# Kernel tuning notes

Measured on AMD Instinct MI355X. Metric: run time of the kernel, lower is better.

## Reference

```python
import jax, jax.numpy as jnp
import numpy as np

D_MODEL = 1024
NUM_HEADS = 16
HEAD_DIM = D_MODEL // NUM_HEADS


def setup_inputs() -> dict:
    key = jax.random.key(0)
    ks = jax.random.split(key, 9)
    B, S = 2, 2048
    s = 1.0 / np.sqrt(D_MODEL)
    inp = {
        "x": jax.random.normal(ks[0], (B, S, D_MODEL), dtype=jnp.float32),
        "Wq": jax.random.normal(ks[1], (D_MODEL, D_MODEL), dtype=jnp.float32) * s,
        "bq": jnp.zeros((D_MODEL,), dtype=jnp.float32),
        "Wk": jax.random.normal(ks[2], (D_MODEL, D_MODEL), dtype=jnp.float32) * s,
        "bk": jnp.zeros((D_MODEL,), dtype=jnp.float32),
        "Wv": jax.random.normal(ks[3], (D_MODEL, D_MODEL), dtype=jnp.float32) * s,
        "bv": jnp.zeros((D_MODEL,), dtype=jnp.float32),
        "Wo": jax.random.normal(ks[4], (D_MODEL, D_MODEL), dtype=jnp.float32) * s,
        "bo": jnpp if False else jnp.zeros((D_MODEL,), dtype=jnp.float32),
    }
    return inp


def reference(x, Wq, bq, Wk, bk, Wv, bv, Wo, bo):
    B, S, D = x.shape
    H, hd = NUM_HEADS, HEAD_DIM
    # QKV projections (Linear: x @ W^T + b), split into heads -> [B,H,S,hd]
    q = (x @ Wq.T + bq).reshape(B, S, H, hd).transpose(0, 2, 1, 3)
    k = (x @ Wk.T + bk).reshape(B, S, H, hd).transpose(0, 2, 1, 3)
    v = (x @ Wv.T + bv).reshape(B, S, H, hd).transpose(0, 2, 1, 3)
    # scores [B,H,S,S]
    scores = jnp.einsum('bhqd,bhkd->bhqk', q, k) / jnp.sqrt(jnp.float32(hd))
    p = jax.nn.softmax(scores, axis=-1)
    out = jnp.einsum('bhqk,bhkd->bhqd', p, v)  # [B,H,S,hd]
    out = out.transpose(0, 2, 1, 3).reshape(B, S, D)
    return out @ Wo.T + bo
```

## Files before the change

kernel.cpp:

```cpp
#include <hip/hip_runtime.h>
#include <hip/hip_bf16.h>
#include <math.h>

typedef __bf16 bf16;
typedef unsigned short u16;
typedef __bf16 bf16x8 __attribute__((ext_vector_type(8)));
typedef __bf16 bf16x4 __attribute__((ext_vector_type(4)));
typedef short  s16x4  __attribute__((ext_vector_type(4)));
typedef float  f32x4  __attribute__((ext_vector_type(4)));

#define D_MODEL 1024
#define NHEAD   16
#define HD      64
#define BATCH   2
#define SEQ     2048
#define MTOT    (BATCH*SEQ)

#define EXPSCALE 0.18033688011116016f

__device__ __forceinline__ void async16(const void* g, void* l) {
    __builtin_amdgcn_global_load_lds(
        (__attribute__((address_space(1))) unsigned int*)g,
        (__attribute__((address_space(3))) unsigned int*)l,
        16, 0, 0);
}

__device__ __forceinline__ f32x4 mfma16(s16x4 a, s16x4 b, f32x4 c) {
    return __builtin_amdgcn_mfma_f32_16x16x16bf16_1k(a, b, c, 0, 0, 0);
}

__global__ __launch_bounds__(256) void cast_kernel(
    const float* __restrict__ x,
    const float* __restrict__ wq, const float* __restrict__ wk,
    const float* __restrict__ wv, const float* __restrict__ wo,
    bf16* __restrict__ xb, bf16* __restrict__ wqb, bf16* __restrict__ wkb,
    bf16* __restrict__ wvb, bf16* __restrict__ wob)
{
    const int z = blockIdx.y;
    const float* src;
    bf16* dst;
    int n;
    if (z == 0)      { src = x;  dst = xb;  n = MTOT * D_MODEL; }
    else if (z == 1) { src = wq; dst = wqb; n = D_MODEL * D_MODEL; }
    else if (z == 2) { src = wk; dst = wkb; n = D_MODEL * D_MODEL; }
    else if (z == 3) { src = wv; dst = wvb; n = D_MODEL * D_MODEL; }
    else             { src = wo; dst = wob; n = D_MODEL * D_MODEL; }

    int i = (blockIdx.x * 256 + threadIdx.x) * 8;
    if (i >= n) return;
    float4 a = *(const float4*)(src + i);
    float4 b = *(const float4*)(src + i + 4);
    bf16x8 o;
    o[0] = (bf16)a.x; o[1] = (bf16)a.y; o[2] = (bf16)a.z; o[3] = (bf16)a.w;
    o[4] = (bf16)b.x; o[5] = (bf16)b.y; o[6] = (bf16)b.z; o[7] = (bf16)b.w;
    *(bf16x8*)(dst + i) = o;
}

__device__ __forceinline__ void gemm_core(const bf16* __restrict__ A,
                                          const bf16* __restrict__ W,
                                          int m0, int n0,
                                          f32x4 acc[4][4],
                                          u16* lA, u16* lB)
{
    const int tid  = threadIdx.x;
    const int lane = tid & 63;
    const int wave = tid >> 6;
    const int wr   = wave >> 1;
    const int wc   = wave & 1;
    const int fr   = lane & 15;
    const int quad = lane >> 4;

    #pragma unroll
    for (int mi = 0; mi < 4; ++mi)
        #pragma unroll
        for (int ni = 0; ni < 4; ++ni)
            #pragma unroll
            for (int e = 0; e < 4; ++e)
                acc[mi][ni][e] = 0.0f;

    const int row = tid >> 3;
    const int ca  = ((tid & 7) ^ (row & 7)) * 8;
    const bf16* gA[4];
    const bf16* gB[4];
    u16 *sA[4], *sB[4];
    #pragma unroll
    for (int c = 0; c < 4; ++c) {
        int slot = tid + c * 256;
        int r    = row + c * 32;
        gA[c] = A + (size_t)(m0 + r) * 1024 + ca;
        gB[c] = W + (size_t)(n0 + r) * 1024 + ca;
        sA[c] = lA + (size_t)slot * 8;
        sB[c] = lB + (size_t)slot * 8;
    }

    for (int kt = 0; kt < 1024 / 64; ++kt) {
        __syncthreads();
        #pragma unroll
        for (int c = 0; c < 4; ++c) {
            async16(gA[c] + kt * 64, sA[c]);
            async16(gB[c] + kt * 64, sB[c]);
        }
        __syncthreads();

        #pragma unroll
        for (int ks = 0; ks < 2; ++ks) {
            const int sa = ((ks * 4 + quad) ^ (fr & 7)) * 8;
            bf16x8 af[4], bfm[4];
            #pragma unroll
            for (int mi = 0; mi < 4; ++mi)
                af[mi] = *(const bf16x8*)(lA + (wr * 64 + mi * 16 + fr) * 64 + sa);
            #pragma unroll
            for (int ni = 0; ni < 4; ++ni)
                bfm[ni] = *(const bf16x8*)(lB + (wc * 64 + ni * 16 + fr) * 64 + sa);

            #pragma unroll
            for (int mi = 0; mi < 4; ++mi)
                #pragma unroll
                for (int ni = 0; ni < 4; ++ni)
                    acc[mi][ni] = __builtin_amdgcn_mfma_f32_16x16x32_bf16(
                        af[mi], bfm[ni], acc[mi][ni], 0, 0, 0);
        }
    }
}

__global__ __launch_bounds__(256) void qkv_kernel(
    const bf16* __restrict__ x,
    const bf16* __restrict__ Wq, const bf16* __restrict__ Wk, const bf16* __restrict__ Wv,
    const float* __restrict__ bq, const float* __restrict__ bk, const float* __restrict__ bv,
    bf16* __restrict__ Q, bf16* __restrict__ K, bf16* __restrict__ Vt)
{
    __shared__ __align__(16) u16 lA[128 * 64];
    __shared__ __align__(16) u16 lB[128 * 64];

    const int z = blockIdx.z;
    int m0, n0;
    const bf16 *mA, *mB;
    const float* bias;
    if (z == 2) {
        mA = Wv; mB = x; bias = bv;
        m0 = blockIdx.y * 128;
        n0 = blockIdx.x * 128;
    } else {
        mA = x;  mB = (z == 0) ? Wq : Wk; bias = (z == 0) ? bq : bk;
        m0 = blockIdx.x * 128;
        n0 = blockIdx.y * 128;
    }

    f32x4 acc[4][4];
    gemm_core(mA, mB, m0, n0, acc, lA, lB);

    const int lane = threadIdx.x & 63;
    const int wave = threadIdx.x >> 6;
    const int wr = wave >> 1, wc = wave & 1;
    const int col = lane & 15, quad = lane >> 4;

    if (z == 2) {
        #pragma unroll
        for (int mi = 0; mi < 4; ++mi) {
            #pragma unroll
            for (int ni = 0; ni < 4; ++ni) {
                #pragma unroll
                for (int r = 0; r < 4; ++r) {
                    int f = m0 + wr * 64 + mi * 16 + quad * 4 + r;
                    int t = n0 + wc * 64 + ni * 16 + col;
                    float v = acc[mi][ni][r] + bias[f];
                    int b = t >> 11, s = t & 2047;
                    int h = f >> 6,  d = f & 63;
                    Vt[((size_t)(b * NHEAD + h) * HD + d) * SEQ + s] = (bf16)v;
                }
            }
        }
    } else {
        const float qs = (z == 0) ? EXPSCALE : 1.0f;
        bf16* o = (z == 0) ? Q : K;
        #pragma unroll
        for (int mi = 0; mi < 4; ++mi) {
            #pragma unroll
            for (int ni = 0; ni < 4; ++ni) {
                #pragma unroll
                for (int r = 0; r < 4; ++r) {
                    int m = m0 + wr * 64 + mi * 16 + quad * 4 + r;
                    int n = n0 + wc * 64 + ni * 16 + col;
                    float v = (acc[mi][ni][r] + bias[n]) * qs;
                    int b = m >> 11, s = m & 2047;
                    int h = n >> 6,  d = n & 63;
                    o[((size_t)(b * NHEAD + h) * SEQ + s) * HD + d] = (bf16)v;
                }
            }
        }
    }
}

__global__ __launch_bounds__(256, 4) void attn_kernel(
    const bf16* __restrict__ Q, const bf16* __restrict__ K,
    const bf16* __restrict__ Vt, bf16* __restrict__ O)
{
    __shared__ __align__(16) u16 lK[128 * 64];
    __shared__ __align__(16) u16 lV[64 * 128];

    const int tid  = threadIdx.x;
    const int lane = tid & 63;
    const int wave = tid >> 6;
    const int col  = lane & 15;
    const int quad = lane >> 4;
    const int bh   = blockIdx.x;
    const int q0   = blockIdx.y * 64;

    const bf16* Qh = Q  + (size_t)bh * SEQ * HD;
    const bf16* Kh = K  + (size_t)bh * SEQ * HD;
    const bf16* Vh = Vt + (size_t)bh * HD * SEQ;

    bf16x8 qf[2];
    #pragma unroll
    for (int ks = 0; ks < 2; ++ks)
        qf[ks] = *(const bf16x8*)(
            Qh + (size_t)(q0 + wave * 16 + col) * HD + ks * 32 + quad * 8);

    f32x4 acc_o[4];
    #pragma unroll
    for (int nd = 0; nd < 4; ++nd)
        #pragma unroll
        for (int e = 0; e < 4; ++e) acc_o[nd][e] = 0.0f;
    float rs = 0.0f;
    const f32x4 zero4 = {0.0f, 0.0f, 0.0f, 0.0f};

    const int krow = tid >> 3;
    const int kca  = ((tid & 7) ^ (krow & 7)) * 8;
    const int vrow = tid >> 4;
    const int vblk = tid & 15;
    const int vca  = ((((vblk & 7) ^ (vrow & 7)) | (vblk & 8))) * 8;
    const bf16* gK[4];
    const bf16* gV[4];
    u16 *sK[4], *sV[4];
    #pragma unroll
    for (int c = 0; c < 4; ++c) {
        int slot = tid + c * 256;
        gK[c] = Kh + (size_t)(krow + c * 32) * HD + kca;
        gV[c] = Vh + (size_t)(vrow + c * 16) * SEQ + vca;
        sK[c] = lK + (size_t)slot * 8;
        sV[c] = lV + (size_t)slot * 8;
    }

    for (int jt = 0; jt < SEQ / 128; ++jt) {
        __syncthreads();
        #pragma unroll
        for (int c = 0; c < 4; ++c) {
            async16(gK[c] + (size_t)jt * 128 * HD, sK[c]);
            async16(gV[c] + jt * 128, sV[c]);
        }
        __syncthreads();

        s16x4 pb[8];
        #pragma unroll
        for (int nj = 0; nj < 8; ++nj) {
            const u16* kr = lK + (nj * 16 + col) * 64;
            bf16x8 kf0 = *(const bf16x8*)(kr + ((0 + quad) ^ (col & 7)) * 8);
            bf16x8 kf1 = *(const bf16x8*)(kr + ((4 + quad) ^ (col & 7)) * 8);
            f32x4 sc = __builtin_amdgcn_mfma_f32_16x16x32_bf16(kf0, qf[0], zero4, 0, 0, 0);
            sc = __builtin_amdgcn_mfma_f32_16x16x32_bf16(kf1, qf[1], sc, 0, 0, 0);
            float p0 = __builtin_amdgcn_exp2f(sc[0]);
            float p1 = __builtin_amdgcn_exp2f(sc[1]);
            float p2 = __builtin_amdgcn_exp2f(sc[2]);
            float p3 = __builtin_amdgcn_exp2f(sc[3]);
            rs += (p0 + p1) + (p2 + p3);
            bf16x4 t;
            t[0] = (bf16)p0; t[1] = (bf16)p1; t[2] = (bf16)p2; t[3] = (bf16)p3;
            pb[nj] = __builtin_bit_cast(s16x4, t);
        }

        #pragma unroll
        for (int nj = 0; nj < 8; ++nj) {
            #pragma unroll
            for (int nd = 0; nd < 4; ++nd) {
                int row = nd * 16 + col;
                int jb  = 2 * nj + (quad >> 1);
                int ph  = ((jb & 7) ^ (row & 7)) | (jb & 8);
                s16x4 vb = *(const s16x4*)(lV + row * 128 + ph * 8 + (quad & 1) * 4);
                acc_o[nd] = mfma16(pb[nj], vb, acc_o[nd]);
            }
        }
    }

    const int b = bh >> 4, h = bh & 15;
    float v = rs;
    v += __shfl_xor(v, 16);
    v += __shfl_xor(v, 32);
    float inv = 1.0f / v;
    float invr[4];
    #pragma unroll
    for (int r = 0; r < 4; ++r)
        invr[r] = __shfl(inv, quad * 4 + r);
    #pragma unroll
    for (int nd = 0; nd < 4; ++nd) {
        #pragma unroll
        for (int r = 0; r < 4; ++r) {
            int srow = q0 + wave * 16 + quad * 4 + r;
            int d    = nd * 16 + col;
            float o  = acc_o[nd][r] * invr[r];
            O[((size_t)(b * SEQ + srow)) * D_MODEL + h * HD + d] = (bf16)o;
        }
    }
}

__global__ __launch_bounds__(256) void oproj_kernel(
    const bf16* __restrict__ A, const bf16* __restrict__ Wo,
    const float* __restrict__ bo, float* __restrict__ out)
{
    __shared__ __align__(16) u16 lA[128 * 32];
    __shared__ __align__(16) u16 lB[64 * 32];

    const int m0 = blockIdx.x * 128;
    const int n0 = blockIdx.y * 64;

    const int tid  = threadIdx.x;
    const int lane = tid & 63;
    const int wave = tid >> 6;
    const int wr   = wave >> 1;
    const int wc   = wave & 1;
    const int fr   = lane & 15;
    const int quad = lane >> 4;
    const int sa   = (quad ^ (fr & 3)) * 8;

    f32x4 acc[4][2];
    #pragma unroll
    for (int mi = 0; mi < 4; ++mi)
        #pragma unroll
        for (int ni = 0; ni < 2; ++ni)
            #pragma unroll
            for (int e = 0; e < 4; ++e)
                acc[mi][ni][e] = 0.0f;

    const int row0 = tid >> 2;
    const int row1 = row0 + 64;
    const int ca   = ((tid & 3) ^ (row0 & 3)) * 8;
    const bf16* gA0 = A  + (size_t)(m0 + row0) * 1024 + ca;
    const bf16* gA1 = A  + (size_t)(m0 + row1) * 1024 + ca;
    const bf16* gB0 = Wo + (size_t)(n0 + row0) * 1024 + ca;
    u16* sA0 = lA + (size_t)tid * 8;
    u16* sA1 = lA + (size_t)(tid + 256) * 8;
    u16* sB0 = lB + (size_t)tid * 8;

    for (int kt = 0; kt < 1024 / 32; ++kt) {
        __syncthreads();
        async16(gA0 + kt * 32, sA0);
        async16(gA1 + kt * 32, sA1);
        async16(gB0 + kt * 32, sB0);
        __syncthreads();

        bf16x8 af[4], bfm[2];
        #pragma unroll
        for (int mi = 0; mi < 4; ++mi)
            af[mi] = *(const bf16x8*)(lA + (wr * 64 + mi * 16 + fr) * 32 + sa);
        #pragma unroll
        for (int ni = 0; ni < 2; ++ni)
            bfm[ni] = *(const bf16x8*)(lB + (wc * 32 + ni * 16 + fr) * 32 + sa);

        #pragma unroll
        for (int mi = 0; mi < 4; ++mi)
            #pragma unroll
            for (int ni = 0; ni < 2; ++ni)
                acc[mi][ni] = __builtin_amdgcn_mfma_f32_16x16x32_bf16(
                    af[mi], bfm[ni], acc[mi][ni], 0, 0, 0);
    }

    const int col = fr;
    #pragma unroll
    for (int mi = 0; mi < 4; ++mi) {
        #pragma unroll
        for (int ni = 0; ni < 2; ++ni) {
            #pragma unroll
            for (int r = 0; r < 4; ++r) {
                int m = m0 + wr * 64 + mi * 16 + quad * 4 + r;
                int n = n0 + wc * 32 + ni * 16 + col;
                out[(size_t)m * D_MODEL + n] = acc[mi][ni][r] + bo[n];
            }
        }
    }
}

extern "C" void kernel_launch(void* const* d_in, const int* in_sizes, int n_in,
                              void* d_out, int out_size, void* d_ws, size_t ws_size,
                              hipStream_t stream)
{
    const float* x  = (const float*)d_in[0];
    const float* Wq = (const float*)d_in[1];
    const float* bq = (const float*)d_in[2];
    const float* Wk = (const float*)d_in[3];
    const float* bk = (const float*)d_in[4];
    const float* Wv = (const float*)d_in[5];
    const float* bv = (const float*)d_in[6];
    const float* Wo = (const float*)d_in[7];
    const float* bo = (const float*)d_in[8];
    float* out = (float*)d_out;

    char* ws = (char*)d_ws;
    const size_t XSZ = (size_t)MTOT * D_MODEL * sizeof(bf16);
    const size_t WSZ = (size_t)D_MODEL * D_MODEL * sizeof(bf16);
    bf16* wqb = (bf16*)(ws);
    bf16* wkb = (bf16*)(ws + WSZ);
    bf16* wvb = (bf16*)(ws + 2 * WSZ);
    bf16* wob = (bf16*)(ws + 3 * WSZ);
    bf16* xb  = (bf16*)(ws + 4 * WSZ);
    bf16* Qb  = (bf16*)(ws + 4 * WSZ + XSZ);
    bf16* Kb  = (bf16*)(ws + 4 * WSZ + 2 * XSZ);
    bf16* Vt  = (bf16*)(ws + 4 * WSZ + 3 * XSZ);
    bf16* At  = (bf16*)(ws + 4 * WSZ + 4 * XSZ);

    cast_kernel<<<dim3((MTOT * D_MODEL) / (256 * 8), 5), 256, 0, stream>>>(
        x, Wq, Wk, Wv, Wo, xb, wqb, wkb, wvb, wob);

    qkv_kernel<<<dim3(32, 8, 3), 256, 0, stream>>>(
        xb, wqb, wkb, wvb, bq, bk, bv, Qb, Kb, Vt);

    attn_kernel<<<dim3(BATCH * NHEAD, SEQ / 64), 256, 0, stream>>>(Qb, Kb, Vt, At);

    oproj_kernel<<<dim3(MTOT / 128, D_MODEL / 64), 256, 0, stream>>>(At, wob, bo, out);
}
```

Measured before the change: 201.2 us.

## Shrink attention KV tile to 64 and deepen o-proj K tile to 64

```diff
diff --git a/kernel.cpp b/kernel.cpp
--- a/kernel.cpp
+++ b/kernel.cpp
@@ -195,8 +195,8 @@
     const bf16* __restrict__ Q, const bf16* __restrict__ K,
     const bf16* __restrict__ Vt, bf16* __restrict__ O)
 {
-    __shared__ __align__(16) u16 lK[128 * 64];
-    __shared__ __align__(16) u16 lV[64 * 128];
+    __shared__ __align__(16) u16 lK[64 * 64];
+    __shared__ __align__(16) u16 lV[64 * 64];
 
     const int tid  = threadIdx.x;
     const int lane = tid & 63;
@@ -224,44 +224,48 @@
     float rs = 0.0f;
     const f32x4 zero4 = {0.0f, 0.0f, 0.0f, 0.0f};
 
-    const int krow = tid >> 3;
-    const int kca  = ((tid & 7) ^ (krow & 7)) * 8;
-    const int vrow = tid >> 4;
-    const int vblk = tid & 15;
-    const int vca  = ((((vblk & 7) ^ (vrow & 7)) | (vblk & 8))) * 8;
-    const bf16* gK[4];
-    const bf16* gV[4];
-    u16 *sK[4], *sV[4];
-    #pragma unroll
-    for (int c = 0; c < 4; ++c) {
-        int slot = tid + c * 256;
-        gK[c] = Kh + (size_t)(krow + c * 32) * HD + kca;
-        gV[c] = Vh + (size_t)(vrow + c * 16) * SEQ + vca;
-        sK[c] = lK + (size_t)slot * 8;
-        sV[c] = lV + (size_t)slot * 8;
-    }
-
-    for (int jt = 0; jt < SEQ / 128; ++jt) {
-        __syncthreads();
-        #pragma unroll
-        for (int c = 0; c < 4; ++c) {
-            async16(gK[c] + (size_t)jt * 128 * HD, sK[c]);
-            async16(gV[c] + jt * 128, sV[c]);
-        }
-        __syncthreads();
-
-        s16x4 pb[8];
-        #pragma unroll
-        for (int nj = 0; nj < 8; ++nj) {
-            const u16* kr = lK + (nj * 16 + col) * 64;
-            bf16x8 kf0 = *(const bf16x8*)(kr + ((0 + quad) ^ (col & 7)) * 8);
-            bf16x8 kf1 = *(const bf16x8*)(kr + ((4 + quad) ^ (col & 7)) * 8);
-            f32x4 sc = __builtin_amdgcn_mfma_f32_16x16x32_bf16(kf0, qf[0], zero4, 0, 0, 0);
-            sc = __builtin_amdgcn_mfma_f32_16x16x32_bf16(kf1, qf[1], sc, 0, 0, 0);
-            float p0 = __builtin_amdgcn_exp2f(sc[0]);
-            float p1 = __builtin_amdgcn_exp2f(sc[1]);
-            float p2 = __builtin_amdgcn_exp2f(sc[2]);
-            float p3 = __builtin_amdgcn_exp2f(sc[3]);
+    const int r0 = tid >> 3;
+    const int r1 = r0 + 32;
+    const int g0 = (((tid & 7) ^ (r0 & 7))) * 8;
+    const int g1 = (((tid & 7) ^ (r1 & 7))) * 8;
+    const bf16* gK0 = Kh + (size_t)r0 * HD + g0;
+    const bf16* gK1 = Kh + (size_t)r1 * HD + g1;
+    const bf16* gV0 = Vh + (size_t)r0 * SEQ + g0;
+    const bf16* gV1 = Vh + (size_t)r1 * SEQ + g1;
+    u16* sK0 = lK + (size_t)tid * 8;
+    u16* sK1 = lK + (size_t)(tid + 256) * 8;
+    u16* sV0 = lV + (size_t)tid * 8;
+    u16* sV1 = lV + (size_t)(tid + 256) * 8;
+
+    for (int jt = 0; jt < SEQ / 64; ++jt) {
+        __syncthreads();
+        async16(gK0 + (size_t)jt * 64 * HD, sK0);
+        async16(gK1 + (size_t)jt * 64 * HD, sK1);
+        async16(gV0 + jt * 64, sV0);
+        async16(gV1 + jt * 64, sV1);
+        __syncthreads();
+
+        f32x4 sc[4];
+        #pragma unroll
+        for (int nj = 0; nj < 4; ++nj) {
+            bf16x8 kf0 = *(const bf16x8*)(
+                lK + (nj * 16 + col) * 64 + ((0 + quad) ^ (col & 7)) * 8);
+            sc[nj] = __builtin_amdgcn_mfma_f32_16x16x32_bf16(kf0, qf[0], zero4, 0, 0, 0);
+        }
+        #pragma unroll
+        for (int nj = 0; nj < 4; ++nj) {
+            bf16x8 kf1 = *(const bf16x8*)(
+                lK + (nj * 16 + col) * 64 + ((4 + quad) ^ (col & 7)) * 8);
+            sc[nj] = __builtin_amdgcn_mfma_f32_16x16x32_bf16(kf1, qf[1], sc[nj], 0, 0, 0);
+        }
+
+        s16x4 pb[4];
+        #pragma unroll
+        for (int nj = 0; nj < 4; ++nj) {
+            float p0 = __builtin_amdgcn_exp2f(sc[nj][0]);
+            float p1 = __builtin_amdgcn_exp2f(sc[nj][1]);
+            float p2 = __builtin_amdgcn_exp2f(sc[nj][2]);
+            float p3 = __builtin_amdgcn_exp2f(sc[nj][3]);
             rs += (p0 + p1) + (p2 + p3);
             bf16x4 t;
             t[0] = (bf16)p0; t[1] = (bf16)p1; t[2] = (bf16)p2; t[3] = (bf16)p3;
@@ -269,13 +273,12 @@
         }
 
         #pragma unroll
-        for (int nj = 0; nj < 8; ++nj) {
+        for (int nj = 0; nj < 4; ++nj) {
             #pragma unroll
             for (int nd = 0; nd < 4; ++nd) {
                 int row = nd * 16 + col;
-                int jb  = 2 * nj + (quad >> 1);
-                int ph  = ((jb & 7) ^ (row & 7)) | (jb & 8);
-                s16x4 vb = *(const s16x4*)(lV + row * 128 + ph * 8 + (quad & 1) * 4);
+                int jb  = (2 * nj + (quad >> 1)) ^ (row & 7);
+                s16x4 vb = *(const s16x4*)(lV + row * 64 + jb * 8 + (quad & 1) * 4);
                 acc_o[nd] = mfma16(pb[nj], vb, acc_o[nd]);
             }
         }
@@ -306,8 +309,8 @@
     const bf16* __restrict__ A, const bf16* __restrict__ Wo,
     const float* __restrict__ bo, float* __restrict__ out)
 {
-    __shared__ __align__(16) u16 lA[128 * 32];
-    __shared__ __align__(16) u16 lB[64 * 32];
+    __shared__ __align__(16) u16 lA[128 * 64];
+    __shared__ __align__(16) u16 lB[64 * 64];
 
     const int m0 = blockIdx.x * 128;
     const int n0 = blockIdx.y * 64;
@@ -319,7 +322,6 @@
     const int wc   = wave & 1;
     const int fr   = lane & 15;
     const int quad = lane >> 4;
-    const int sa   = (quad ^ (fr & 3)) * 8;
 
     f32x4 acc[4][2];
     #pragma unroll
@@ -330,37 +332,51 @@
             for (int e = 0; e < 4; ++e)
                 acc[mi][ni][e] = 0.0f;
 
-    const int row0 = tid >> 2;
-    const int row1 = row0 + 64;
-    const int ca   = ((tid & 3) ^ (row0 & 3)) * 8;
-    const bf16* gA0 = A  + (size_t)(m0 + row0) * 1024 + ca;
-    const bf16* gA1 = A  + (size_t)(m0 + row1) * 1024 + ca;
-    const bf16* gB0 = Wo + (size_t)(n0 + row0) * 1024 + ca;
-    u16* sA0 = lA + (size_t)tid * 8;
-    u16* sA1 = lA + (size_t)(tid + 256) * 8;
-    u16* sB0 = lB + (size_t)tid * 8;
-
-    for (int kt = 0; kt < 1024 / 32; ++kt) {
-        __syncthreads();
-        async16(gA0 + kt * 32, sA0);
-        async16(gA1 + kt * 32, sA1);
-        async16(gB0 + kt * 32, sB0);
-        __syncthreads();
-
-        bf16x8 af[4], bfm[2];
-        #pragma unroll
-        for (int mi = 0; mi < 4; ++mi)
-            af[mi] = *(const bf16x8*)(lA + (wr * 64 + mi * 16 + fr) * 32 + sa);
-        #pragma unroll
-        for (int ni = 0; ni < 2; ++ni)
-            bfm[ni] = *(const bf16x8*)(lB + (wc * 32 + ni * 16 + fr) * 32 + sa);
-
-        #pragma unroll
-        for (int mi = 0; mi < 4; ++mi)
+    const int row = tid >> 3;
+    const int ca  = ((tid & 7) ^ (row & 7)) * 8;
+    const bf16* gA[4];
+    u16* sA[4];
+    #pragma unroll
+    for (int c = 0; c < 4; ++c) {
+        int slot = tid + c * 256;
+        gA[c] = A + (size_t)(m0 + row + c * 32) * 1024 + ca;
+        sA[c] = lA + (size_t)slot * 8;
+    }
+    const bf16* gB[2];
+    u16* sB[2];
+    #pragma unroll
+    for (int c = 0; c < 2; ++c) {
+        int slot = tid + c * 256;
+        gB[c] = Wo + (size_t)(n0 + row + c * 32) * 1024 + ca;
+        sB[c] = lB + (size_t)slot * 8;
+    }
+
+    for (int kt = 0; kt < 1024 / 64; ++kt) {
+        __syncthreads();
+        #pragma unroll
+        for (int c = 0; c < 4; ++c) async16(gA[c] + kt * 64, sA[c]);
+        #pragma unroll
+        for (int c = 0; c < 2; ++c) async16(gB[c] + kt * 64, sB[c]);
+        __syncthreads();
+
+        #pragma unroll
+        for (int ks = 0; ks < 2; ++ks) {
+            const int sa = ((ks * 4 + quad) ^ (fr & 7)) * 8;
+            bf16x8 af[4], bfm[2];
+            #pragma unroll
+            for (int mi = 0; mi < 4; ++mi)
+                af[mi] = *(const bf16x8*)(lA + (wr * 64 + mi * 16 + fr) * 64 + sa);
             #pragma unroll
             for (int ni = 0; ni < 2; ++ni)
-                acc[mi][ni] = __builtin_amdgcn_mfma_f32_16x16x32_bf16(
-                    af[mi], bfm[ni], acc[mi][ni], 0, 0, 0);
+                bfm[ni] = *(const bf16x8*)(lB + (wc * 32 + ni * 16 + fr) * 64 + sa);
+
+            #pragma unroll
+            for (int mi = 0; mi < 4; ++mi)
+                #pragma unroll
+                for (int ni = 0; ni < 2; ++ni)
+                    acc[mi][ni] = __builtin_amdgcn_mfma_f32_16x16x32_bf16(
+                        af[mi], bfm[ni], acc[mi][ni], 0, 0, 0);
+        }
     }
 
     const int col = fr;
```

Result: faster. 196.3 us (-2.4%).
